# Kernel optimization log

Hardware: AMD Instinct MI355X
Metric: run time of the kernel (lower is better)

Reference implementation:

```python
import jax, jax.numpy as jnp
import numpy as np

# sean_choice hyperparameters (param tuple: alpha_by_beta, beta, gamma, delta_by_gamma, zeta, _)
ALPHA_BY_BETA = 10.0
BETA = 20.0
GAMMA = 0.25
DELTA_BY_GAMMA = 0.2
ZETA = 0.1

BATCH, N_VAR, N_CLAUSE, N_SAT = 16, 100000, 400000, 3


def setup_inputs() -> dict:
    key = jax.random.key(0)
    k1, k2, k3, k4, k5 = jax.random.split(key, 5)
    v = jax.random.uniform(k1, (BATCH, N_VAR), jnp.float32, -1.0, 1.0)
    input_idx = jax.random.randint(k2, (BATCH, N_CLAUSE, N_SAT), 0, N_VAR, dtype=jnp.int32)
    input_sign = (2 * jax.random.randint(k3, (BATCH, N_CLAUSE, N_SAT), 0, 2) - 1).astype(jnp.float32)
    xl = 1.0 + jax.random.uniform(k4, (BATCH, N_CLAUSE), jnp.float32)          # clamped to [1, max_xl]
    xs = jax.random.uniform(k5, (BATCH, N_CLAUSE), jnp.float32)                 # clamped to [0, 1]
    alpha_multiplier = jnp.ones((BATCH, N_CLAUSE), jnp.float32)
    return {"v": v, "input_idx": input_idx, "input_sign": input_sign,
            "xl": xl, "xs": xs, "alpha_multiplier": alpha_multiplier}


def reference(v, input_idx, input_sign, xl, xs, alpha_multiplier):
    batch, n_clause, n_sat = input_idx.shape
    b = jnp.arange(batch)[:, None, None]
    # gather per-clause literal voltages and apply literal polarity: [B, C, S]
    v_input = v[b, input_idx] * input_sign
    # top-2 literal values per clause
    v_top, v_idx = jax.lax.top_k(v_input, 2)
    v_top = (1.0 - v_top) / 2.0
    C = v_top[:, :, 0]                                   # clause violation in [0,1]
    # G: broadcast C, except the argmax slot gets the runner-up value
    argmax_mask = jnp.arange(n_sat)[None, None, :] == v_idx[:, :, 0:1]
    G = jnp.where(argmax_mask, v_top[:, :, 1:2], C[:, :, None]) * (xl * xs)[:, :, None]
    # R: nonzero only at the argmax slot (sean_choice scaling)
    R = jnp.where(argmax_mask, C[:, :, None], 0.0) * ((1.0 + ZETA * xl) * (1.0 - xs))[:, :, None]
    dv = -(G + R) * input_sign
    thresh = DELTA_BY_GAMMA * GAMMA
    dxl = jnp.where(C >= thresh,
                    -(ALPHA_BY_BETA * BETA * alpha_multiplier * (C - thresh)),
                    -(10.0 * (C - thresh) * (xl - 1.0)))
    dxs = -(BETA * (C - GAMMA))
    # scatter_add dv back into v.grad along the variable axis
    v_grad = jnp.zeros_like(v).at[
        jnp.arange(batch)[:, None], input_idx.reshape(batch, -1)
    ].add(dv.reshape(batch, -1))
    return C, v_grad, dxl, dxs
```

## Files before the change

kernel.cpp:

```cpp
#include <hip/hip_runtime.h>
#include <stdint.h>

#define BATCH    16
#define N_VAR    100000
#define N_CLAUSE 400000
#define NR       3
#define RS       33336
#define QPB      (N_CLAUSE / 4)
#define QPP      (2 * QPB)
#define CAP      408000

#define QSCALE2  8192.0f
#define QINV2    (1.0f / 8192.0f)

typedef int      vi4 __attribute__((ext_vector_type(4)));
typedef float    vf4 __attribute__((ext_vector_type(4)));
typedef uint32_t vu4 __attribute__((ext_vector_type(4)));

__device__ __forceinline__ void do_clause2(
    float g0, float g1, float g2, float s0, float s1, float s2,
    float xlv, float xsv, float amv,
    float& Cv, float& dxlv, float& dxsv,
    float& dv0, float& dv1, float& dv2)
{
    const float a0 = g0 * s0, a1 = g1 * s1, a2 = g2 * s2;
    const float m = fmaxf(a0, fmaxf(a1, a2));
    const int am = (a0 == m) ? 0 : ((a1 == m) ? 1 : 2);
    const float sec = (am == 0) ? fmaxf(a1, a2)
                    : (am == 1) ? fmaxf(a0, a2)
                                : fmaxf(a0, a1);
    const float C  = 0.5f * (1.0f - m);
    const float t1 = 0.5f * (1.0f - sec);
    const float gam  = t1 * (xlv * xsv) + C * ((1.0f + 0.1f * xlv) * (1.0f - xsv));
    const float goth = C * (xlv * xsv);
    dv0 = -((am == 0) ? gam : goth) * s0;
    dv1 = -((am == 1) ? gam : goth) * s1;
    dv2 = -((am == 2) ? gam : goth) * s2;
    Cv = C;
    const float d = C - 0.05f;
    dxlv = (C >= 0.05f) ? -(200.0f * amv * d) : -(10.0f * d * (xlv - 1.0f));
    dxsv = -(20.0f * (C - 0.25f));
}

__device__ __forceinline__ void pack2(int gidx, float dv, uint32_t& w, int& r) {
    r = (gidx >= RS) + (gidx >= 2 * RS);
    int q = __float2int_rn(dv * QSCALE2);
    q = max(-32767, min(32767, q));
    w = ((uint32_t)(gidx - r * RS) << 16) | ((uint32_t)q & 0xFFFFu);
}

__global__ __launch_bounds__(256) void phaseA_kernel(
    const float* __restrict__ v,
    const int*   __restrict__ idx,
    const float* __restrict__ sgn,
    const float* __restrict__ xl,
    const float* __restrict__ xs,
    const float* __restrict__ amul,
    float*    __restrict__ C_out,
    float*    __restrict__ dxl,
    float*    __restrict__ dxs,
    uint32_t* __restrict__ buckets,
    int*      __restrict__ gcnt)
{
    __shared__ int      lcnt[6];
    __shared__ int      scan[7];
    __shared__ int      gbase[6];
    __shared__ uint32_t stage[12 * 256];

    const int p   = blockIdx.x & 7;
    const int inr = blockIdx.x >> 3;
    const int t   = inr * 256 + (int)threadIdx.x;
    const bool active = (t < QPP);

    if (threadIdx.x < 6) lcnt[threadIdx.x] = 0;
    __syncthreads();

    int b = p * 2;
    uint32_t w0=0,w1=0,w2=0,w3=0,w4=0,w5=0,w6=0,w7=0,w8=0,w9=0,w10=0,w11=0;
    int r0=0,r1=0,r2=0,r3=0,r4=0,r5=0,r6=0,r7=0,r8=0,r9=0,r10=0,r11=0;
    int cA = 0, cB = 0, cC = 0;
    int bl = 0;

    if (active) {
        b = p * 2 + t / QPB;
        bl = (b & 1) * 3;
        const int q = b * QPB + t % QPB;
        const long e  = 12L * q;
        const int  ci = q * 4;

        const vi4 ia = __builtin_nontemporal_load((const vi4*)(idx + e));
        const vi4 ib = __builtin_nontemporal_load((const vi4*)(idx + e + 4));
        const vi4 ic = __builtin_nontemporal_load((const vi4*)(idx + e + 8));
        const vf4 sa = __builtin_nontemporal_load((const vf4*)(sgn + e));
        const vf4 sb = __builtin_nontemporal_load((const vf4*)(sgn + e + 4));
        const vf4 sc = __builtin_nontemporal_load((const vf4*)(sgn + e + 8));
        const vf4 xlv = __builtin_nontemporal_load((const vf4*)(xl + ci));
        const vf4 xsv = __builtin_nontemporal_load((const vf4*)(xs + ci));
        const vf4 amv = __builtin_nontemporal_load((const vf4*)(amul + ci));

        const float* __restrict__ vb = v + (long)b * N_VAR;
        const float g00 = vb[ia.x], g01 = vb[ia.y], g02 = vb[ia.z];
        const float g10 = vb[ia.w], g11 = vb[ib.x], g12 = vb[ib.y];
        const float g20 = vb[ib.z], g21 = vb[ib.w], g22 = vb[ic.x];
        const float g30 = vb[ic.y], g31 = vb[ic.z], g32 = vb[ic.w];

        float C0,C1,C2,C3, L0,L1,L2,L3, S0,S1,S2,S3;
        float d0,d1,d2,d3,d4,d5,d6,d7,d8,d9,d10,d11;
        do_clause2(g00,g01,g02, sa.x,sa.y,sa.z, xlv.x,xsv.x,amv.x, C0,L0,S0, d0,d1,d2);
        do_clause2(g10,g11,g12, sa.w,sb.x,sb.y, xlv.y,xsv.y,amv.y, C1,L1,S1, d3,d4,d5);
        do_clause2(g20,g21,g22, sb.z,sb.w,sc.x, xlv.z,xsv.z,amv.z, C2,L2,S2, d6,d7,d8);
        do_clause2(g30,g31,g32, sc.y,sc.z,sc.w, xlv.w,xsv.w,amv.w, C3,L3,S3, d9,d10,d11);

        vf4 Cv; Cv.x = C0; Cv.y = C1; Cv.z = C2; Cv.w = C3;
        vf4 dl; dl.x = L0; dl.y = L1; dl.z = L2; dl.w = L3;
        vf4 ds; ds.x = S0; ds.y = S1; ds.z = S2; ds.w = S3;
        __builtin_nontemporal_store(Cv, (vf4*)(C_out + ci));
        __builtin_nontemporal_store(dl, (vf4*)(dxl   + ci));
        __builtin_nontemporal_store(ds, (vf4*)(dxs   + ci));

        pack2(ia.x, d0,  w0,  r0);  pack2(ia.y, d1,  w1,  r1);  pack2(ia.z, d2,  w2,  r2);
        pack2(ia.w, d3,  w3,  r3);  pack2(ib.x, d4,  w4,  r4);  pack2(ib.y, d5,  w5,  r5);
        pack2(ib.z, d6,  w6,  r6);  pack2(ib.w, d7,  w7,  r7);  pack2(ic.x, d8,  w8,  r8);
        pack2(ic.y, d9,  w9,  r9);  pack2(ic.z, d10, w10, r10); pack2(ic.w, d11, w11, r11);

        cA = (r0==0)+(r1==0)+(r2==0)+(r3==0)+(r4==0)+(r5==0)
           + (r6==0)+(r7==0)+(r8==0)+(r9==0)+(r10==0)+(r11==0);
        cB = (r0==1)+(r1==1)+(r2==1)+(r3==1)+(r4==1)+(r5==1)
           + (r6==1)+(r7==1)+(r8==1)+(r9==1)+(r10==1)+(r11==1);
        cC = 12 - cA - cB;
    }

    int tA = 0, tB = 0, tC = 0;
    if (active) {
        tA = atomicAdd(&lcnt[bl + 0], cA);
        tB = atomicAdd(&lcnt[bl + 1], cB);
        tC = atomicAdd(&lcnt[bl + 2], cC);
    }
    __syncthreads();

    if (threadIdx.x == 0) {
        scan[0] = 0;
        #pragma unroll
        for (int k = 0; k < 6; ++k) {
            scan[k + 1] = scan[k] + lcnt[k];
            const int bk = p * 2 + (k >= 3);
            const int rr = k - (k >= 3) * 3;
            gbase[k] = lcnt[k] ? atomicAdd(&gcnt[bk * 3 + rr], lcnt[k]) : 0;
        }
    }
    __syncthreads();

    if (active) {
        int LA = scan[bl + 0] + tA;
        int LB = scan[bl + 1] + tB;
        int LC = scan[bl + 2] + tC;
        #define EMIT(W, R) { if ((R)==0) stage[LA++] = (W); \
                             else if ((R)==1) stage[LB++] = (W); \
                             else stage[LC++] = (W); }
        EMIT(w0,r0)  EMIT(w1,r1)  EMIT(w2,r2)  EMIT(w3,r3)
        EMIT(w4,r4)  EMIT(w5,r5)  EMIT(w6,r6)  EMIT(w7,r7)
        EMIT(w8,r8)  EMIT(w9,r9)  EMIT(w10,r10) EMIT(w11,r11)
        #undef EMIT
    }
    __syncthreads();

    const int tot = scan[6];
    for (int j = threadIdx.x; j < tot; j += 256) {
        int k = (j >= scan[1]) + (j >= scan[2]) + (j >= scan[3])
              + (j >= scan[4]) + (j >= scan[5]);
        const int bk = p * 2 + (k >= 3);
        const int rr = k - (k >= 3) * 3;
        const int dpos = gbase[k] + (j - scan[k]);
        if (dpos < CAP)
            __builtin_nontemporal_store(stage[j],
                buckets + (size_t)(bk * 3 + rr) * CAP + dpos);
    }
}

__global__ __launch_bounds__(1024) void phaseB_kernel(
    const uint32_t* __restrict__ buckets,
    const int*      __restrict__ gcnt,
    float* __restrict__ partial,
    int nC)
{
    __shared__ int acc[RS];

    const int blk = blockIdx.x;
    const int r  = blk % NR;
    const int b2 = (blk / NR) % BATCH;
    const int c  = blk / (NR * BATCH);

    for (int k = threadIdx.x; k < RS; k += 1024) acc[k] = 0;
    __syncthreads();

    int n = gcnt[b2 * 3 + r];
    if (n > CAP) n = CAP;
    const uint32_t* __restrict__ bkt = buckets + (size_t)(b2 * 3 + r) * CAP;
    const int start = (int)(((long)n * c / nC) & ~3L);
    const int end   = (c == nC - 1) ? n : (int)(((long)n * (c + 1) / nC) & ~3L);
    const int len   = end - start;
    const uint32_t* __restrict__ src = bkt + start;

    #define PROC(W) atomicAdd(&acc[(W) >> 16], (int)(short)((W) & 0xFFFFu));
    const int ngrp = len >> 3;
    for (int t = threadIdx.x; t < ngrp; t += 1024) {
        const vu4 e0 = __builtin_nontemporal_load((const vu4*)(src + 8 * t));
        const vu4 e1 = __builtin_nontemporal_load((const vu4*)(src + 8 * t + 4));
        PROC(e0.x) PROC(e0.y) PROC(e0.z) PROC(e0.w)
        PROC(e1.x) PROC(e1.y) PROC(e1.z) PROC(e1.w)
    }
    for (int u = (ngrp << 3) + (int)threadIdx.x; u < len; u += 1024) {
        const uint32_t e0 = __builtin_nontemporal_load(src + u);
        PROC(e0)
    }
    #undef PROC
    __syncthreads();

    const int lo = r * RS;
    const int kend = min((int)RS, N_VAR - lo);
    float* __restrict__ p = partial + ((size_t)c * BATCH + b2) * N_VAR + lo;
    for (int k = threadIdx.x; 4 * k < kend; k += 1024) {
        vf4 f;
        f.x = (float)acc[4 * k + 0] * QINV2;
        f.y = (float)acc[4 * k + 1] * QINV2;
        f.z = (float)acc[4 * k + 2] * QINV2;
        f.w = (float)acc[4 * k + 3] * QINV2;
        __builtin_nontemporal_store(f, (vf4*)(p + 4 * k));
    }
}

__global__ __launch_bounds__(256) void phaseC_kernel(
    const float* __restrict__ partial,
    float* __restrict__ vgrad,
    int nC)
{
    const int total4 = BATCH * (N_VAR / 4);
    const int t = blockIdx.x * blockDim.x + threadIdx.x;
    if (t >= total4) return;
    const int b  = t / (N_VAR / 4);
    const int k4 = t % (N_VAR / 4);
    vf4 s; s.x = 0.f; s.y = 0.f; s.z = 0.f; s.w = 0.f;
    for (int c = 0; c < nC; ++c) {
        const vf4 p = __builtin_nontemporal_load(
            (const vf4*)&partial[((size_t)c * BATCH + b) * N_VAR + (size_t)k4 * 4]);
        s.x += p.x; s.y += p.y; s.z += p.z; s.w += p.w;
    }
    *(vf4*)&vgrad[(size_t)b * N_VAR + (size_t)k4 * 4] = s;
}

__global__ __launch_bounds__(256) void fallback_kernel(
    const float* __restrict__ v,
    const int*   __restrict__ idx,
    const float* __restrict__ sgn,
    const float* __restrict__ xl,
    const float* __restrict__ xs,
    const float* __restrict__ amul,
    float* __restrict__ C_out,
    float* __restrict__ vgrad,
    float* __restrict__ dxl,
    float* __restrict__ dxs,
    int total)
{
    const int stride = gridDim.x * blockDim.x;
    for (int i = blockIdx.x * blockDim.x + threadIdx.x; i < total; i += stride) {
        const int b = i / N_CLAUSE;
        const long base = 3L * i;
        const int i0 = idx[base], i1 = idx[base + 1], i2 = idx[base + 2];
        const float s0 = sgn[base], s1 = sgn[base + 1], s2 = sgn[base + 2];
        const float* vb = v + (long)b * N_VAR;
        const float a0 = vb[i0] * s0;
        const float a1 = vb[i1] * s1;
        const float a2 = vb[i2] * s2;
        const float m = fmaxf(a0, fmaxf(a1, a2));
        const int am = (a0 == m) ? 0 : ((a1 == m) ? 1 : 2);
        const float sec = (am == 0) ? fmaxf(a1, a2)
                        : (am == 1) ? fmaxf(a0, a2)
                                    : fmaxf(a0, a1);
        const float C  = 0.5f * (1.0f - m);
        const float t1 = 0.5f * (1.0f - sec);
        const float xlv = xl[i];
        const float xsv = xs[i];
        const float gam  = t1 * (xlv * xsv) + C * ((1.0f + 0.1f * xlv) * (1.0f - xsv));
        const float goth = C * (xlv * xsv);
        float* gb = vgrad + (long)b * N_VAR;
        atomicAdd(gb + i0, -((am == 0) ? gam : goth) * s0);
        atomicAdd(gb + i1, -((am == 1) ? gam : goth) * s1);
        atomicAdd(gb + i2, -((am == 2) ? gam : goth) * s2);
        C_out[i] = C;
        const float d = C - 0.05f;
        dxl[i] = (C >= 0.05f) ? -(200.0f * amul[i] * d)
                              : -(10.0f * d * (xlv - 1.0f));
        dxs[i] = -(20.0f * (C - 0.25f));
    }
}

extern "C" void kernel_launch(void* const* d_in, const int* in_sizes, int n_in,
                              void* d_out, int out_size, void* d_ws, size_t ws_size,
                              hipStream_t stream) {
    const float* v    = (const float*)d_in[0];
    const int*   idx  = (const int*)  d_in[1];
    const float* sgn  = (const float*)d_in[2];
    const float* xl   = (const float*)d_in[3];
    const float* xs   = (const float*)d_in[4];
    const float* amul = (const float*)d_in[5];

    float* out   = (float*)d_out;
    float* C_out = out;
    float* vgrad = C_out + (size_t)BATCH * N_CLAUSE;
    float* dxl   = vgrad + (size_t)BATCH * N_VAR;
    float* dxs   = dxl   + (size_t)BATCH * N_CLAUSE;

    const size_t cntBytes = 256;
    const size_t bktBytes = (size_t)BATCH * NR * CAP * 4;
    const size_t perC     = (size_t)BATCH * N_VAR * sizeof(float);

    int nC = 0;
    if (ws_size >= cntBytes + bktBytes + perC) {
        const size_t fit = (ws_size - cntBytes - bktBytes) / perC;
        nC = (fit >= 5) ? 5 : (int)fit;
    }

    if (nC >= 1) {
        int*      gcnt    = (int*)d_ws;
        uint32_t* buckets = (uint32_t*)((char*)d_ws + cntBytes);
        float*    partial = (float*)((char*)d_ws + cntBytes + bktBytes);

        (void)hipMemsetAsync(d_ws, 0, cntBytes, stream);

        const int gridA = 8 * ((QPP + 255) / 256);
        phaseA_kernel<<<gridA, 256, 0, stream>>>(
            v, idx, sgn, xl, xs, amul, C_out, dxl, dxs, buckets, gcnt);

        phaseB_kernel<<<nC * BATCH * NR, 1024, 0, stream>>>(buckets, gcnt, partial, nC);

        const int total4 = BATCH * (N_VAR / 4);
        phaseC_kernel<<<(total4 + 255) / 256, 256, 0, stream>>>(partial, vgrad, nC);
    } else {
        (void)hipMemsetAsync(vgrad, 0, sizeof(float) * (size_t)BATCH * N_VAR, stream);
        fallback_kernel<<<2048, 256, 0, stream>>>(v, idx, sgn, xl, xs, amul,
                                                  C_out, vgrad, dxl, dxs,
                                                  BATCH * N_CLAUSE);
    }
}
```

Measured before the change: 193.5 us.

## Cache first third of batch voltages in LDS with persistent phase A blocks

```diff
diff --git a/kernel.cpp b/kernel.cpp
--- a/kernel.cpp
+++ b/kernel.cpp
@@ -7,8 +7,13 @@
 #define NR       3
 #define RS       33336
 #define QPB      (N_CLAUSE / 4)
-#define QPP      (2 * QPB)
 #define CAP      408000
+
+#define TPB_A    512
+#define SLOTS    32
+#define STRIDE_A (SLOTS * TPB_A)
+#define NIT      ((QPB + STRIDE_A - 1) / STRIDE_A)
+#define VC       33792
 
 #define QSCALE2  8192.0f
 #define QINV2    (1.0f / 8192.0f)
@@ -49,7 +54,7 @@
     w = ((uint32_t)(gidx - r * RS) << 16) | ((uint32_t)q & 0xFFFFu);
 }
 
-__global__ __launch_bounds__(256) void phaseA_kernel(
+__global__ __launch_bounds__(512) void phaseA_kernel(
     const float* __restrict__ v,
     const int*   __restrict__ idx,
     const float* __restrict__ sgn,
@@ -62,118 +67,126 @@
     uint32_t* __restrict__ buckets,
     int*      __restrict__ gcnt)
 {
-    __shared__ int      lcnt[6];
-    __shared__ int      scan[7];
-    __shared__ int      gbase[6];
-    __shared__ uint32_t stage[12 * 256];
-
-    const int p   = blockIdx.x & 7;
-    const int inr = blockIdx.x >> 3;
-    const int t   = inr * 256 + (int)threadIdx.x;
-    const bool active = (t < QPP);
-
-    if (threadIdx.x < 6) lcnt[threadIdx.x] = 0;
-    __syncthreads();
-
-    int b = p * 2;
-    uint32_t w0=0,w1=0,w2=0,w3=0,w4=0,w5=0,w6=0,w7=0,w8=0,w9=0,w10=0,w11=0;
-    int r0=0,r1=0,r2=0,r3=0,r4=0,r5=0,r6=0,r7=0,r8=0,r9=0,r10=0,r11=0;
-    int cA = 0, cB = 0, cC = 0;
-    int bl = 0;
-
-    if (active) {
-        b = p * 2 + t / QPB;
-        bl = (b & 1) * 3;
-        const int q = b * QPB + t % QPB;
-        const long e  = 12L * q;
-        const int  ci = q * 4;
-
-        const vi4 ia = __builtin_nontemporal_load((const vi4*)(idx + e));
-        const vi4 ib = __builtin_nontemporal_load((const vi4*)(idx + e + 4));
-        const vi4 ic = __builtin_nontemporal_load((const vi4*)(idx + e + 8));
-        const vf4 sa = __builtin_nontemporal_load((const vf4*)(sgn + e));
-        const vf4 sb = __builtin_nontemporal_load((const vf4*)(sgn + e + 4));
-        const vf4 sc = __builtin_nontemporal_load((const vf4*)(sgn + e + 8));
-        const vf4 xlv = __builtin_nontemporal_load((const vf4*)(xl + ci));
-        const vf4 xsv = __builtin_nontemporal_load((const vf4*)(xs + ci));
-        const vf4 amv = __builtin_nontemporal_load((const vf4*)(amul + ci));
-
-        const float* __restrict__ vb = v + (long)b * N_VAR;
-        const float g00 = vb[ia.x], g01 = vb[ia.y], g02 = vb[ia.z];
-        const float g10 = vb[ia.w], g11 = vb[ib.x], g12 = vb[ib.y];
-        const float g20 = vb[ib.z], g21 = vb[ib.w], g22 = vb[ic.x];
-        const float g30 = vb[ic.y], g31 = vb[ic.z], g32 = vb[ic.w];
-
-        float C0,C1,C2,C3, L0,L1,L2,L3, S0,S1,S2,S3;
-        float d0,d1,d2,d3,d4,d5,d6,d7,d8,d9,d10,d11;
-        do_clause2(g00,g01,g02, sa.x,sa.y,sa.z, xlv.x,xsv.x,amv.x, C0,L0,S0, d0,d1,d2);
-        do_clause2(g10,g11,g12, sa.w,sb.x,sb.y, xlv.y,xsv.y,amv.y, C1,L1,S1, d3,d4,d5);
-        do_clause2(g20,g21,g22, sb.z,sb.w,sc.x, xlv.z,xsv.z,amv.z, C2,L2,S2, d6,d7,d8);
-        do_clause2(g30,g31,g32, sc.y,sc.z,sc.w, xlv.w,xsv.w,amv.w, C3,L3,S3, d9,d10,d11);
-
-        vf4 Cv; Cv.x = C0; Cv.y = C1; Cv.z = C2; Cv.w = C3;
-        vf4 dl; dl.x = L0; dl.y = L1; dl.z = L2; dl.w = L3;
-        vf4 ds; ds.x = S0; ds.y = S1; ds.z = S2; ds.w = S3;
-        __builtin_nontemporal_store(Cv, (vf4*)(C_out + ci));
-        __builtin_nontemporal_store(dl, (vf4*)(dxl   + ci));
-        __builtin_nontemporal_store(ds, (vf4*)(dxs   + ci));
-
-        pack2(ia.x, d0,  w0,  r0);  pack2(ia.y, d1,  w1,  r1);  pack2(ia.z, d2,  w2,  r2);
-        pack2(ia.w, d3,  w3,  r3);  pack2(ib.x, d4,  w4,  r4);  pack2(ib.y, d5,  w5,  r5);
-        pack2(ib.z, d6,  w6,  r6);  pack2(ib.w, d7,  w7,  r7);  pack2(ic.x, d8,  w8,  r8);
-        pack2(ic.y, d9,  w9,  r9);  pack2(ic.z, d10, w10, r10); pack2(ic.w, d11, w11, r11);
-
-        cA = (r0==0)+(r1==0)+(r2==0)+(r3==0)+(r4==0)+(r5==0)
-           + (r6==0)+(r7==0)+(r8==0)+(r9==0)+(r10==0)+(r11==0);
-        cB = (r0==1)+(r1==1)+(r2==1)+(r3==1)+(r4==1)+(r5==1)
-           + (r6==1)+(r7==1)+(r8==1)+(r9==1)+(r10==1)+(r11==1);
-        cC = 12 - cA - cB;
-    }
-
-    int tA = 0, tB = 0, tC = 0;
-    if (active) {
-        tA = atomicAdd(&lcnt[bl + 0], cA);
-        tB = atomicAdd(&lcnt[bl + 1], cB);
-        tC = atomicAdd(&lcnt[bl + 2], cC);
-    }
-    __syncthreads();
-
-    if (threadIdx.x == 0) {
-        scan[0] = 0;
-        #pragma unroll
-        for (int k = 0; k < 6; ++k) {
-            scan[k + 1] = scan[k] + lcnt[k];
-            const int bk = p * 2 + (k >= 3);
-            const int rr = k - (k >= 3) * 3;
-            gbase[k] = lcnt[k] ? atomicAdd(&gcnt[bk * 3 + rr], lcnt[k]) : 0;
+    __shared__ float    vcache[VC];
+    __shared__ int      lcnt[3];
+    __shared__ int      scan[4];
+    __shared__ int      gbase[3];
+    __shared__ uint32_t stage[12 * TPB_A];
+
+    const int p    = blockIdx.x & 7;
+    const int slot = blockIdx.x >> 3;
+    const int tid  = (int)threadIdx.x;
+
+    for (int half = 0; half < 2; ++half) {
+        const int b = p * 2 + half;
+        const float* __restrict__ vb = v + (size_t)b * N_VAR;
+
+        __syncthreads();
+        for (int k = tid; k < VC / 4; k += TPB_A)
+            ((vf4*)vcache)[k] = ((const vf4*)vb)[k];
+        __syncthreads();
+
+        for (int it = 0; it < NIT; ++it) {
+            const int q0 = it * STRIDE_A + slot * TPB_A + tid;
+            const bool active = q0 < QPB;
+            if (tid < 3) lcnt[tid] = 0;
+            __syncthreads();
+
+            uint32_t w0=0,w1=0,w2=0,w3=0,w4=0,w5=0,w6=0,w7=0,w8=0,w9=0,w10=0,w11=0;
+            int r0=0,r1=0,r2=0,r3=0,r4=0,r5=0,r6=0,r7=0,r8=0,r9=0,r10=0,r11=0;
+            int cA = 0, cB = 0, cC = 0;
+
+            if (active) {
+                const int q  = b * QPB + q0;
+                const long e = 12L * q;
+                const int ci = q * 4;
+
+                const vi4 ia = __builtin_nontemporal_load((const vi4*)(idx + e));
+                const vi4 ib = __builtin_nontemporal_load((const vi4*)(idx + e + 4));
+                const vi4 ic = __builtin_nontemporal_load((const vi4*)(idx + e + 8));
+                const vf4 sa = __builtin_nontemporal_load((const vf4*)(sgn + e));
+                const vf4 sb = __builtin_nontemporal_load((const vf4*)(sgn + e + 4));
+                const vf4 sc = __builtin_nontemporal_load((const vf4*)(sgn + e + 8));
+                const vf4 xlv = __builtin_nontemporal_load((const vf4*)(xl + ci));
+                const vf4 xsv = __builtin_nontemporal_load((const vf4*)(xs + ci));
+                const vf4 amv = __builtin_nontemporal_load((const vf4*)(amul + ci));
+
+                float g00,g01,g02,g10,g11,g12,g20,g21,g22,g30,g31,g32;
+                #define GATH(DST, U) { const int u_ = (U); \
+                    if (u_ < VC) DST = vcache[u_]; else DST = vb[u_]; }
+                GATH(g00, ia.x) GATH(g01, ia.y) GATH(g02, ia.z)
+                GATH(g10, ia.w) GATH(g11, ib.x) GATH(g12, ib.y)
+                GATH(g20, ib.z) GATH(g21, ib.w) GATH(g22, ic.x)
+                GATH(g30, ic.y) GATH(g31, ic.z) GATH(g32, ic.w)
+                #undef GATH
+
+                float C0,C1,C2,C3, L0,L1,L2,L3, S0,S1,S2,S3;
+                float d0,d1,d2,d3,d4,d5,d6,d7,d8,d9,d10,d11;
+                do_clause2(g00,g01,g02, sa.x,sa.y,sa.z, xlv.x,xsv.x,amv.x, C0,L0,S0, d0,d1,d2);
+                do_clause2(g10,g11,g12, sa.w,sb.x,sb.y, xlv.y,xsv.y,amv.y, C1,L1,S1, d3,d4,d5);
+                do_clause2(g20,g21,g22, sb.z,sb.w,sc.x, xlv.z,xsv.z,amv.z, C2,L2,S2, d6,d7,d8);
+                do_clause2(g30,g31,g32, sc.y,sc.z,sc.w, xlv.w,xsv.w,amv.w, C3,L3,S3, d9,d10,d11);
+
+                vf4 Cv; Cv.x = C0; Cv.y = C1; Cv.z = C2; Cv.w = C3;
+                vf4 dl; dl.x = L0; dl.y = L1; dl.z = L2; dl.w = L3;
+                vf4 ds; ds.x = S0; ds.y = S1; ds.z = S2; ds.w = S3;
+                __builtin_nontemporal_store(Cv, (vf4*)(C_out + ci));
+                __builtin_nontemporal_store(dl, (vf4*)(dxl   + ci));
+                __builtin_nontemporal_store(ds, (vf4*)(dxs   + ci));
+
+                pack2(ia.x, d0,  w0,  r0);  pack2(ia.y, d1,  w1,  r1);  pack2(ia.z, d2,  w2,  r2);
+                pack2(ia.w, d3,  w3,  r3);  pack2(ib.x, d4,  w4,  r4);  pack2(ib.y, d5,  w5,  r5);
+                pack2(ib.z, d6,  w6,  r6);  pack2(ib.w, d7,  w7,  r7);  pack2(ic.x, d8,  w8,  r8);
+                pack2(ic.y, d9,  w9,  r9);  pack2(ic.z, d10, w10, r10); pack2(ic.w, d11, w11, r11);
+
+                cA = (r0==0)+(r1==0)+(r2==0)+(r3==0)+(r4==0)+(r5==0)
+                   + (r6==0)+(r7==0)+(r8==0)+(r9==0)+(r10==0)+(r11==0);
+                cB = (r0==1)+(r1==1)+(r2==1)+(r3==1)+(r4==1)+(r5==1)
+                   + (r6==1)+(r7==1)+(r8==1)+(r9==1)+(r10==1)+(r11==1);
+                cC = 12 - cA - cB;
+            }
+
+            int tA = 0, tB = 0, tC = 0;
+            if (active) {
+                tA = atomicAdd(&lcnt[0], cA);
+                tB = atomicAdd(&lcnt[1], cB);
+                tC = atomicAdd(&lcnt[2], cC);
+            }
+            __syncthreads();
+
+            if (tid == 0) {
+                scan[0] = 0;
+                #pragma unroll
+                for (int k = 0; k < 3; ++k) {
+                    scan[k + 1] = scan[k] + lcnt[k];
+                    gbase[k] = lcnt[k] ? atomicAdd(&gcnt[b * 3 + k], lcnt[k]) : 0;
+                }
+            }
+            __syncthreads();
+
+            if (active) {
+                int LA = scan[0] + tA;
+                int LB = scan[1] + tB;
+                int LC = scan[2] + tC;
+                #define EMIT(W, R) { if ((R)==0) stage[LA++] = (W); \
+                                     else if ((R)==1) stage[LB++] = (W); \
+                                     else stage[LC++] = (W); }
+                EMIT(w0,r0)  EMIT(w1,r1)  EMIT(w2,r2)  EMIT(w3,r3)
+                EMIT(w4,r4)  EMIT(w5,r5)  EMIT(w6,r6)  EMIT(w7,r7)
+                EMIT(w8,r8)  EMIT(w9,r9)  EMIT(w10,r10) EMIT(w11,r11)
+                #undef EMIT
+            }
+            __syncthreads();
+
+            const int tot = scan[3];
+            for (int j = tid; j < tot; j += TPB_A) {
+                const int k = (j >= scan[1]) + (j >= scan[2]);
+                const int dpos = gbase[k] + (j - scan[k]);
+                if (dpos < CAP)
+                    __builtin_nontemporal_store(stage[j],
+                        buckets + (size_t)(b * 3 + k) * CAP + dpos);
+            }
         }
-    }
-    __syncthreads();
-
-    if (active) {
-        int LA = scan[bl + 0] + tA;
-        int LB = scan[bl + 1] + tB;
-        int LC = scan[bl + 2] + tC;
-        #define EMIT(W, R) { if ((R)==0) stage[LA++] = (W); \
-                             else if ((R)==1) stage[LB++] = (W); \
-                             else stage[LC++] = (W); }
-        EMIT(w0,r0)  EMIT(w1,r1)  EMIT(w2,r2)  EMIT(w3,r3)
-        EMIT(w4,r4)  EMIT(w5,r5)  EMIT(w6,r6)  EMIT(w7,r7)
-        EMIT(w8,r8)  EMIT(w9,r9)  EMIT(w10,r10) EMIT(w11,r11)
-        #undef EMIT
-    }
-    __syncthreads();
-
-    const int tot = scan[6];
-    for (int j = threadIdx.x; j < tot; j += 256) {
-        int k = (j >= scan[1]) + (j >= scan[2]) + (j >= scan[3])
-              + (j >= scan[4]) + (j >= scan[5]);
-        const int bk = p * 2 + (k >= 3);
-        const int rr = k - (k >= 3) * 3;
-        const int dpos = gbase[k] + (j - scan[k]);
-        if (dpos < CAP)
-            __builtin_nontemporal_store(stage[j],
-                buckets + (size_t)(bk * 3 + rr) * CAP + dpos);
     }
 }
 
@@ -327,8 +340,7 @@
 
         (void)hipMemsetAsync(d_ws, 0, cntBytes, stream);
 
-        const int gridA = 8 * ((QPP + 255) / 256);
-        phaseA_kernel<<<gridA, 256, 0, stream>>>(
+        phaseA_kernel<<<256, TPB_A, 0, stream>>>(
             v, idx, sgn, xl, xs, amul, C_out, dxl, dxs, buckets, gcnt);
 
         phaseB_kernel<<<nC * BATCH * NR, 1024, 0, stream>>>(buckets, gcnt, partial, nC);
```

Result: slower. 308.7 us (+59.5%).
